# Kernel tuning notes

Measured on AMD Instinct MI355X. Metric: run time of the kernel, lower is better.

The kernel has to match this reference:

```python
import jax, jax.numpy as jnp
import numpy as np

N, E = 50000, 800000
NODE_DIM, HIDDEN, NBASIS = 128, 128, 32


def _mlp(x, w1, b1, w2, b2):
    return jax.nn.silu(x @ w1 + b1) @ w2 + b2


def setup_inputs() -> dict:
    key = jax.random.key(0)
    ks = jax.random.split(key, 16)
    d = {}
    d['h'] = jax.random.normal(ks[0], (N, NODE_DIM), dtype=jnp.float32)
    d['pos'] = jax.random.normal(ks[1], (N, 3), dtype=jnp.float32)
    d['edge_index'] = jax.random.randint(ks[2], (2, E), 0, N, dtype=jnp.int32)
    mlp_in = NODE_DIM * 2 + NBASIS
    def lin(k, fan_in, fan_out):
        bound = 1.0 / np.sqrt(fan_in)
        kw, kb = jax.random.split(k)
        w = jax.random.uniform(kw, (fan_in, fan_out), minval=-bound, maxval=bound, dtype=jnp.float32)
        b = jax.random.uniform(kb, (fan_out,), minval=-bound, maxval=bound, dtype=jnp.float32)
        return w, b
    d['mw1'], d['mb1'] = lin(ks[3], mlp_in, HIDDEN)
    d['mw2'], d['mb2'] = lin(ks[4], HIDDEN, HIDDEN)
    d['nw1'], d['nb1'] = lin(ks[5], NODE_DIM + HIDDEN, HIDDEN)
    d['nw2'], d['nb2'] = lin(ks[6], HIDDEN, NODE_DIM)
    d['cw1'], d['cb1'] = lin(ks[7], HIDDEN, HIDDEN)
    d['cw2'], d['cb2'] = lin(ks[8], HIDDEN, 1)
    return d


def reference(h, pos, edge_index, mw1, mb1, mw2, mb2, nw1, nb1, nw2, nb2, cw1, cb1, cw2, cb2):
    row, col = edge_index[0], edge_index[1]
    # Gaussian smearing constants (start=0, stop=10, num_gaussians=NBASIS)
    offset = jnp.linspace(0.0, 10.0, NBASIS)  # [NBASIS]
    coeff = -0.5 / float(10.0 / (NBASIS - 1)) ** 2

    rel_pos = pos[row] - pos[col]                       # [E, 3]
    sq_dist = jnp.sum(rel_pos ** 2, axis=1, keepdims=True)  # [E, 1]
    dist = jnp.sqrt(sq_dist + 1e-8)                     # [E, 1]
    dist_emb = jnp.exp(coeff * (dist - offset[None, :]) ** 2)  # [E, NBASIS]

    msg_in = jnp.concatenate([h[row], h[col], dist_emb], axis=1)  # [E, 2D+NBASIS]
    messages = _mlp(msg_in, mw1, mb1, mw2, mb2)         # [E, HIDDEN]

    aggr_msgs = jax.ops.segment_sum(messages, row, num_segments=h.shape[0])  # [N, HIDDEN]

    coord_mult = _mlp(messages, cw1, cb1, cw2, cb2)     # [E, 1]
    coord_updates = rel_pos * coord_mult                # [E, 3]
    aggr_coord = jax.ops.segment_sum(coord_updates, row, num_segments=pos.shape[0])
    pos_out = pos + aggr_coord

    node_in = jnp.concatenate([h, aggr_msgs], axis=1)   # [N, D+HIDDEN]
    h_out = h + _mlp(node_in, nw1, nb1, nw2, nb2)
    return (h_out, pos_out)
```

## Files before the change

kernel.cpp:

```cpp
#include <hip/hip_runtime.h>
#include <math.h>

#define N_NODES 50000
#define E_EDGES 800000
#define D 128
#define HID 128
#define NB 32

typedef __attribute__((ext_vector_type(8))) short bf16x8;
typedef __attribute__((ext_vector_type(4))) float f32x4;

#define MW1F 0
#define MW2F 72
#define CW1F 104
#define NW1F 136
#define NW2F 200
#define TOT_KSTEPS 29

__device__ __forceinline__ short f2bf(float f) {
    union { float f; unsigned u; } v; v.f = f;
    unsigned r = v.u + 0x7fffu + ((v.u >> 16) & 1u);
    return (short)(r >> 16);
}
__device__ __forceinline__ float silu_f(float x) { return x / (1.0f + __expf(-x)); }
__device__ __forceinline__ f32x4 splat4(float b) { f32x4 v = {b, b, b, b}; return v; }

__global__ void pack_w(const float* __restrict__ mw1, const float* __restrict__ mw2,
                       const float* __restrict__ cw1, const float* __restrict__ nw1,
                       const float* __restrict__ nw2, short* __restrict__ wp)
{
    const int bid = blockIdx.x;
    const int ks = bid >> 3, nf = bid & 7;
    const int l = threadIdx.x;
    const float* src; int k0;
    if (ks < 9)       { src = mw1; k0 = ks; }
    else if (ks < 13) { src = mw2; k0 = ks - 9; }
    else if (ks < 17) { src = cw1; k0 = ks - 13; }
    else if (ks < 25) { src = nw1; k0 = ks - 17; }
    else              { src = nw2; k0 = ks - 25; }
    bf16x8 pv;
    #pragma unroll
    for (int j = 0; j < 8; ++j)
        pv[j] = f2bf(src[(size_t)(k0 * 32 + (l >> 4) * 8 + j) * 128 + nf * 16 + (l & 15)]);
    *((bf16x8*)wp + (size_t)bid * 64 + l) = pv;
}

#define GEMM2(KSTEPS, STRIDE, WBASE)                                           \
    _Pragma("unroll")                                                          \
    for (int ks = 0; ks < KSTEPS; ++ks) {                                      \
        const int kd = ks * 32 + ag * 8;                                       \
        int b0 = ar * STRIDE + kd * 2;        b0 ^= (ar & 7) << 4;             \
        int b1 = (16 + ar) * STRIDE + kd * 2; b1 ^= (ar & 7) << 4;             \
        bf16x8 a0 = *(const bf16x8*)(sx + b0);                                 \
        bf16x8 a1 = *(const bf16x8*)(sx + b1);                                 \
        const bf16x8* bw = wpv + (size_t)(WBASE + ks * 8) * 64 + l;            \
        _Pragma("unroll")                                                      \
        for (int n = 0; n < 8; ++n) {                                          \
            bf16x8 bb = bw[n * 64];                                            \
            acc0[n] = __builtin_amdgcn_mfma_f32_16x16x32_bf16(a0, bb, acc0[n], 0, 0, 0); \
            acc1[n] = __builtin_amdgcn_mfma_f32_16x16x32_bf16(a1, bb, acc1[n], 0, 0, 0); \
        }                                                                      \
    }

__global__ __launch_bounds__(128, 2) void egnn_edge(
    const float* __restrict__ h, const float* __restrict__ pos,
    const int* __restrict__ ei,
    const float* __restrict__ mb1, const float* __restrict__ mb2,
    const float* __restrict__ cb1, const float* __restrict__ cw2,
    const float* __restrict__ cb2, const short* __restrict__ wp,
    float* __restrict__ aggr_msgs, float* __restrict__ aggr_coord)
{
    __shared__ char sm[2][18432];
    __shared__ int   s_rowm[2][32];
    __shared__ float s_relm[2][32][3];

    const int t = threadIdx.x;
    const int w = t >> 6;
    const int l = t & 63;
    char* sx = sm[w];
    const bf16x8* wpv = (const bf16x8*)wp;
    const int e0 = blockIdx.x * 64 + w * 32;

    {
        const int e_loc = l & 31, half = l >> 5;
        const int ge = e0 + e_loc;
        const int row = ei[ge], col = ei[E_EDGES + ge];
        const float dx = pos[row * 3 + 0] - pos[col * 3 + 0];
        const float dy = pos[row * 3 + 1] - pos[col * 3 + 1];
        const float dz = pos[row * 3 + 2] - pos[col * 3 + 2];
        const float dist = sqrtf(dx * dx + dy * dy + dz * dz + 1e-8f);
        if (half == 0) {
            s_rowm[w][e_loc] = row;
            s_relm[w][e_loc][0] = dx; s_relm[w][e_loc][1] = dy; s_relm[w][e_loc][2] = dz;
        }
        const float GS = 10.0f / 31.0f;
        const float GC = -0.5f / (GS * GS);
        const float* hrow = h + (size_t)row * D;
        const float* hcol = h + (size_t)col * D;
        #pragma unroll
        for (int c = 0; c < 18; ++c) {
            const int k0 = half * 144 + c * 8;
            float v[8];
            if (k0 < 256) {
                const float* src = (k0 < 128) ? (hrow + k0) : (hcol + (k0 - 128));
                float4 va = *(const float4*)src;
                float4 vb = *(const float4*)(src + 4);
                v[0] = va.x; v[1] = va.y; v[2] = va.z; v[3] = va.w;
                v[4] = vb.x; v[5] = vb.y; v[6] = vb.z; v[7] = vb.w;
            } else {
                #pragma unroll
                for (int j = 0; j < 8; ++j) {
                    float dd = dist - (float)(k0 - 256 + j) * GS;
                    v[j] = __expf(GC * dd * dd);
                }
            }
            bf16x8 sv;
            #pragma unroll
            for (int j = 0; j < 8; ++j) sv[j] = f2bf(v[j]);
            int byte = e_loc * 576 + k0 * 2;
            byte ^= (e_loc & 7) << 4;
            *(bf16x8*)(sx + byte) = sv;
        }
    }
    asm volatile("s_waitcnt lgkmcnt(0)" ::: "memory");

    const int ar = l & 15, ag = l >> 4;
    f32x4 acc0[8], acc1[8];

    #pragma unroll
    for (int n = 0; n < 8; ++n) {
        float b = mb1[n * 16 + ar];
        acc0[n] = splat4(b); acc1[n] = splat4(b);
    }
    GEMM2(9, 576, MW1F)

    #pragma unroll
    for (int m = 0; m < 2; ++m)
        #pragma unroll
        for (int n = 0; n < 8; ++n)
            #pragma unroll
            for (int r = 0; r < 4; ++r) {
                float x = (m == 0) ? acc0[n][r] : acc1[n][r];
                const int rw = m * 16 + ag * 4 + r;
                const int cl = n * 16 + ar;
                int byte = rw * 256 + cl * 2;
                byte ^= (rw & 7) << 4;
                *(short*)(sx + byte) = f2bf(silu_f(x));
            }
    asm volatile("s_waitcnt lgkmcnt(0)" ::: "memory");

    #pragma unroll
    for (int n = 0; n < 8; ++n) {
        float b = mb2[n * 16 + ar];
        acc0[n] = splat4(b); acc1[n] = splat4(b);
    }
    GEMM2(4, 256, MW2F)

    int grows[2][4];
    #pragma unroll
    for (int m = 0; m < 2; ++m)
        #pragma unroll
        for (int r = 0; r < 4; ++r)
            grows[m][r] = s_rowm[w][m * 16 + ag * 4 + r];

    #pragma unroll
    for (int m = 0; m < 2; ++m)
        #pragma unroll
        for (int n = 0; n < 8; ++n)
            #pragma unroll
            for (int r = 0; r < 4; ++r) {
                float x = (m == 0) ? acc0[n][r] : acc1[n][r];
                const int rw = m * 16 + ag * 4 + r;
                const int cl = n * 16 + ar;
                int byte = rw * 256 + cl * 2;
                byte ^= (rw & 7) << 4;
                *(short*)(sx + byte) = f2bf(x);
                atomicAdd(&aggr_msgs[(size_t)grows[m][r] * D + cl], x);
            }
    asm volatile("s_waitcnt lgkmcnt(0)" ::: "memory");

    #pragma unroll
    for (int n = 0; n < 8; ++n) {
        float b = cb1[n * 16 + ar];
        acc0[n] = splat4(b); acc1[n] = splat4(b);
    }
    GEMM2(4, 256, CW1F)

    float cw2v[8];
    #pragma unroll
    for (int n = 0; n < 8; ++n) cw2v[n] = cw2[n * 16 + ar];
    float p0[4], p1[4];
    #pragma unroll
    for (int r = 0; r < 4; ++r) {
        float s0 = 0.f, s1 = 0.f;
        #pragma unroll
        for (int n = 0; n < 8; ++n) {
            s0 += silu_f(acc0[n][r]) * cw2v[n];
            s1 += silu_f(acc1[n][r]) * cw2v[n];
        }
        p0[r] = s0; p1[r] = s1;
    }
    #pragma unroll
    for (int off = 1; off < 16; off <<= 1) {
        #pragma unroll
        for (int r = 0; r < 4; ++r) {
            p0[r] += __shfl_xor(p0[r], off);
            p1[r] += __shfl_xor(p1[r], off);
        }
    }
    if (ar == 0) {
        const float cb = cb2[0];
        #pragma unroll
        for (int m = 0; m < 2; ++m)
            #pragma unroll
            for (int r = 0; r < 4; ++r) {
                const int el = m * 16 + ag * 4 + r;
                const float mm = ((m == 0) ? p0[r] : p1[r]) + cb;
                const int gr = grows[m][r];
                atomicAdd(&aggr_coord[gr * 3 + 0], s_relm[w][el][0] * mm);
                atomicAdd(&aggr_coord[gr * 3 + 1], s_relm[w][el][1] * mm);
                atomicAdd(&aggr_coord[gr * 3 + 2], s_relm[w][el][2] * mm);
            }
    }
}

__global__ __launch_bounds__(128, 2) void egnn_node(
    const float* __restrict__ h, const float* __restrict__ aggr,
    const float* __restrict__ nb1, const float* __restrict__ nb2,
    const short* __restrict__ wp, float* __restrict__ out)
{
    __shared__ char sm[2][16384];
    const int t = threadIdx.x, w = t >> 6, l = t & 63;
    char* sx = sm[w];
    const bf16x8* wpv = (const bf16x8*)wp;
    const int n0 = blockIdx.x * 64 + w * 32;

    {
        const int n_loc = l & 31, half = l >> 5;
        int gn = n0 + n_loc; if (gn >= N_NODES) gn = N_NODES - 1;
        const float* src = (half == 0) ? (h + (size_t)gn * D) : (aggr + (size_t)gn * D);
        #pragma unroll
        for (int c = 0; c < 16; ++c) {
            float4 va = *(const float4*)(src + c * 8);
            float4 vb = *(const float4*)(src + c * 8 + 4);
            float v[8] = {va.x, va.y, va.z, va.w, vb.x, vb.y, vb.z, vb.w};
            bf16x8 sv;
            #pragma unroll
            for (int j = 0; j < 8; ++j) sv[j] = f2bf(v[j]);
            int byte = n_loc * 512 + (half * 128 + c * 8) * 2;
            byte ^= (n_loc & 7) << 4;
            *(bf16x8*)(sx + byte) = sv;
        }
    }
    asm volatile("s_waitcnt lgkmcnt(0)" ::: "memory");

    const int ar = l & 15, ag = l >> 4;
    f32x4 acc0[8], acc1[8];

    #pragma unroll
    for (int n = 0; n < 8; ++n) {
        float b = nb1[n * 16 + ar];
        acc0[n] = splat4(b); acc1[n] = splat4(b);
    }
    GEMM2(8, 512, NW1F)

    #pragma unroll
    for (int m = 0; m < 2; ++m)
        #pragma unroll
        for (int n = 0; n < 8; ++n)
            #pragma unroll
            for (int r = 0; r < 4; ++r) {
                float x = (m == 0) ? acc0[n][r] : acc1[n][r];
                const int rw = m * 16 + ag * 4 + r;
                const int cl = n * 16 + ar;
                int byte = rw * 256 + cl * 2;
                byte ^= (rw & 7) << 4;
                *(short*)(sx + byte) = f2bf(silu_f(x));
            }
    asm volatile("s_waitcnt lgkmcnt(0)" ::: "memory");

    #pragma unroll
    for (int n = 0; n < 8; ++n) {
        float b = nb2[n * 16 + ar];
        acc0[n] = splat4(b); acc1[n] = splat4(b);
    }
    GEMM2(4, 256, NW2F)

    #pragma unroll
    for (int m = 0; m < 2; ++m)
        #pragma unroll
        for (int n = 0; n < 8; ++n)
            #pragma unroll
            for (int r = 0; r < 4; ++r) {
                const int rw = m * 16 + ag * 4 + r;
                const int gnode = n0 + rw;
                if (gnode < N_NODES) {
                    const int cl = n * 16 + ar;
                    float x = (m == 0) ? acc0[n][r] : acc1[n][r];
                    out[(size_t)gnode * D + cl] = h[(size_t)gnode * D + cl] + x;
                }
            }
}

__global__ void egnn_pos(const float* __restrict__ pos,
                         const float* __restrict__ aggr_coord,
                         float* __restrict__ pout)
{
    int i = blockIdx.x * 256 + threadIdx.x;
    if (i < N_NODES * 3) pout[i] = pos[i] + aggr_coord[i];
}

extern "C" void kernel_launch(void* const* d_in, const int* in_sizes, int n_in,
                              void* d_out, int out_size, void* d_ws, size_t ws_size,
                              hipStream_t stream)
{
    const float* h   = (const float*)d_in[0];
    const float* pos = (const float*)d_in[1];
    const int*   ei  = (const int*)d_in[2];
    const float* mw1 = (const float*)d_in[3];
    const float* mb1 = (const float*)d_in[4];
    const float* mw2 = (const float*)d_in[5];
    const float* mb2 = (const float*)d_in[6];
    const float* nw1 = (const float*)d_in[7];
    const float* nb1 = (const float*)d_in[8];
    const float* nw2 = (const float*)d_in[9];
    const float* nb2 = (const float*)d_in[10];
    const float* cw1 = (const float*)d_in[11];
    const float* cb1 = (const float*)d_in[12];
    const float* cw2 = (const float*)d_in[13];
    const float* cb2 = (const float*)d_in[14];

    float* out        = (float*)d_out;
    float* aggr_msgs  = (float*)d_ws;
    float* aggr_coord = aggr_msgs + (size_t)N_NODES * D;
    short* wpack      = (short*)(aggr_coord + (size_t)N_NODES * 3);

    hipMemsetAsync(d_ws, 0, (size_t)(N_NODES * D + N_NODES * 3) * sizeof(float), stream);

    pack_w<<<TOT_KSTEPS * 8, 64, 0, stream>>>(mw1, mw2, cw1, nw1, nw2, wpack);

    egnn_edge<<<E_EDGES / 64, 128, 0, stream>>>(
        h, pos, ei, mb1, mb2, cb1, cw2, cb2, wpack, aggr_msgs, aggr_coord);

    egnn_node<<<(N_NODES + 63) / 64, 128, 0, stream>>>(
        h, aggr_msgs, nb1, nb2, wpack, out);

    egnn_pos<<<(N_NODES * 3 + 255) / 256, 256, 0, stream>>>(
        pos, aggr_coord, out + (size_t)N_NODES * D);
}
```

Before: 602.2 us.

## Pre-convert h to bf16 and load MFMA A-fragments directly from global

Adds a kernel that converts node features h to bf16 once. The edge kernel then gathers the row and column feature fragments straight into MFMA A registers and computes the Gaussian basis in registers, with no staging of the 288-wide input through LDS. This halves gather bytes and cuts LDS use, which allows 4 waves per block and higher occupancy. The cost is an extra conversion pass, a larger workspace, and uncoalesced 16-byte gathers issued per fragment.

```diff
diff --git a/kernel.cpp b/kernel.cpp
--- a/kernel.cpp
+++ b/kernel.cpp
@@ -43,6 +43,19 @@
     for (int j = 0; j < 8; ++j)
         pv[j] = f2bf(src[(size_t)(k0 * 32 + (l >> 4) * 8 + j) * 128 + nf * 16 + (l & 15)]);
     *((bf16x8*)wp + (size_t)bid * 64 + l) = pv;
+}
+
+__global__ void conv_h(const float* __restrict__ h, short* __restrict__ hb)
+{
+    int i = blockIdx.x * 256 + threadIdx.x;
+    if (i < N_NODES * D / 8) {
+        float4 va = ((const float4*)h)[i * 2];
+        float4 vb = ((const float4*)h)[i * 2 + 1];
+        bf16x8 o;
+        o[0] = f2bf(va.x); o[1] = f2bf(va.y); o[2] = f2bf(va.z); o[3] = f2bf(va.w);
+        o[4] = f2bf(vb.x); o[5] = f2bf(vb.y); o[6] = f2bf(vb.z); o[7] = f2bf(vb.w);
+        ((bf16x8*)hb)[i] = o;
+    }
 }
 
 #define GEMM2(KSTEPS, STRIDE, WBASE)                                           \
@@ -62,69 +75,47 @@
         }                                                                      \
     }
 
-__global__ __launch_bounds__(128, 2) void egnn_edge(
-    const float* __restrict__ h, const float* __restrict__ pos,
+__global__ __launch_bounds__(256, 4) void egnn_edge(
+    const short* __restrict__ hb, const float* __restrict__ pos,
     const int* __restrict__ ei,
     const float* __restrict__ mb1, const float* __restrict__ mb2,
     const float* __restrict__ cb1, const float* __restrict__ cw2,
     const float* __restrict__ cb2, const short* __restrict__ wp,
     float* __restrict__ aggr_msgs, float* __restrict__ aggr_coord)
 {
-    __shared__ char sm[2][18432];
-    __shared__ int   s_rowm[2][32];
-    __shared__ float s_relm[2][32][3];
+    __shared__ char  sm[4][8192];
+    __shared__ int   s_row[4][32], s_col[4][32];
+    __shared__ float s_dist[4][32];
+    __shared__ float s_rel[4][32][3];
 
     const int t = threadIdx.x;
     const int w = t >> 6;
     const int l = t & 63;
     char* sx = sm[w];
     const bf16x8* wpv = (const bf16x8*)wp;
-    const int e0 = blockIdx.x * 64 + w * 32;
-
-    {
-        const int e_loc = l & 31, half = l >> 5;
-        const int ge = e0 + e_loc;
+    const bf16x8* hbv = (const bf16x8*)hb;
+    const int e0 = blockIdx.x * 128 + w * 32;
+
+    if (l < 32) {
+        const int ge = e0 + l;
         const int row = ei[ge], col = ei[E_EDGES + ge];
         const float dx = pos[row * 3 + 0] - pos[col * 3 + 0];
         const float dy = pos[row * 3 + 1] - pos[col * 3 + 1];
         const float dz = pos[row * 3 + 2] - pos[col * 3 + 2];
         const float dist = sqrtf(dx * dx + dy * dy + dz * dz + 1e-8f);
-        if (half == 0) {
-            s_rowm[w][e_loc] = row;
-            s_relm[w][e_loc][0] = dx; s_relm[w][e_loc][1] = dy; s_relm[w][e_loc][2] = dz;
-        }
-        const float GS = 10.0f / 31.0f;
-        const float GC = -0.5f / (GS * GS);
-        const float* hrow = h + (size_t)row * D;
-        const float* hcol = h + (size_t)col * D;
-        #pragma unroll
-        for (int c = 0; c < 18; ++c) {
-            const int k0 = half * 144 + c * 8;
-            float v[8];
-            if (k0 < 256) {
-                const float* src = (k0 < 128) ? (hrow + k0) : (hcol + (k0 - 128));
-                float4 va = *(const float4*)src;
-                float4 vb = *(const float4*)(src + 4);
-                v[0] = va.x; v[1] = va.y; v[2] = va.z; v[3] = va.w;
-                v[4] = vb.x; v[5] = vb.y; v[6] = vb.z; v[7] = vb.w;
-            } else {
-                #pragma unroll
-                for (int j = 0; j < 8; ++j) {
-                    float dd = dist - (float)(k0 - 256 + j) * GS;
-                    v[j] = __expf(GC * dd * dd);
-                }
-            }
-            bf16x8 sv;
-            #pragma unroll
-            for (int j = 0; j < 8; ++j) sv[j] = f2bf(v[j]);
-            int byte = e_loc * 576 + k0 * 2;
-            byte ^= (e_loc & 7) << 4;
-            *(bf16x8*)(sx + byte) = sv;
-        }
+        s_row[w][l] = row; s_col[w][l] = col; s_dist[w][l] = dist;
+        s_rel[w][l][0] = dx; s_rel[w][l][1] = dy; s_rel[w][l][2] = dz;
     }
     asm volatile("s_waitcnt lgkmcnt(0)" ::: "memory");
 
     const int ar = l & 15, ag = l >> 4;
+    const int row0 = s_row[w][ar],      col0 = s_col[w][ar];
+    const int row1 = s_row[w][16 + ar], col1 = s_col[w][16 + ar];
+    const float d0 = s_dist[w][ar], d1 = s_dist[w][16 + ar];
+
+    const float GS = 10.0f / 31.0f;
+    const float GC = -0.5f / (GS * GS);
+
     f32x4 acc0[8], acc1[8];
 
     #pragma unroll
@@ -132,7 +123,32 @@
         float b = mb1[n * 16 + ar];
         acc0[n] = splat4(b); acc1[n] = splat4(b);
     }
-    GEMM2(9, 576, MW1F)
+    #pragma unroll
+    for (int ks = 0; ks < 9; ++ks) {
+        bf16x8 a0, a1;
+        if (ks < 4) {
+            a0 = hbv[(size_t)row0 * 16 + ks * 4 + ag];
+            a1 = hbv[(size_t)row1 * 16 + ks * 4 + ag];
+        } else if (ks < 8) {
+            a0 = hbv[(size_t)col0 * 16 + (ks - 4) * 4 + ag];
+            a1 = hbv[(size_t)col1 * 16 + (ks - 4) * 4 + ag];
+        } else {
+            #pragma unroll
+            for (int j = 0; j < 8; ++j) {
+                const float g = (float)(ag * 8 + j) * GS;
+                const float dd0 = d0 - g, dd1 = d1 - g;
+                a0[j] = f2bf(__expf(GC * dd0 * dd0));
+                a1[j] = f2bf(__expf(GC * dd1 * dd1));
+            }
+        }
+        const bf16x8* bw = wpv + (size_t)(MW1F + ks * 8) * 64 + l;
+        #pragma unroll
+        for (int n = 0; n < 8; ++n) {
+            bf16x8 bb = bw[n * 64];
+            acc0[n] = __builtin_amdgcn_mfma_f32_16x16x32_bf16(a0, bb, acc0[n], 0, 0, 0);
+            acc1[n] = __builtin_amdgcn_mfma_f32_16x16x32_bf16(a1, bb, acc1[n], 0, 0, 0);
+        }
+    }
 
     #pragma unroll
     for (int m = 0; m < 2; ++m)
@@ -161,7 +177,7 @@
     for (int m = 0; m < 2; ++m)
         #pragma unroll
         for (int r = 0; r < 4; ++r)
-            grows[m][r] = s_rowm[w][m * 16 + ag * 4 + r];
+            grows[m][r] = s_row[w][m * 16 + ag * 4 + r];
 
     #pragma unroll
     for (int m = 0; m < 2; ++m)
@@ -217,9 +233,9 @@
                 const int el = m * 16 + ag * 4 + r;
                 const float mm = ((m == 0) ? p0[r] : p1[r]) + cb;
                 const int gr = grows[m][r];
-                atomicAdd(&aggr_coord[gr * 3 + 0], s_relm[w][el][0] * mm);
-                atomicAdd(&aggr_coord[gr * 3 + 1], s_relm[w][el][1] * mm);
-                atomicAdd(&aggr_coord[gr * 3 + 2], s_relm[w][el][2] * mm);
+                atomicAdd(&aggr_coord[gr * 3 + 0], s_rel[w][el][0] * mm);
+                atomicAdd(&aggr_coord[gr * 3 + 1], s_rel[w][el][1] * mm);
+                atomicAdd(&aggr_coord[gr * 3 + 2], s_rel[w][el][2] * mm);
             }
     }
 }
@@ -334,13 +350,15 @@
     float* aggr_msgs  = (float*)d_ws;
     float* aggr_coord = aggr_msgs + (size_t)N_NODES * D;
     short* wpack      = (short*)(aggr_coord + (size_t)N_NODES * 3);
+    short* hb         = wpack + (size_t)TOT_KSTEPS * 8 * 64 * 8;
 
     hipMemsetAsync(d_ws, 0, (size_t)(N_NODES * D + N_NODES * 3) * sizeof(float), stream);
 
     pack_w<<<TOT_KSTEPS * 8, 64, 0, stream>>>(mw1, mw2, cw1, nw1, nw2, wpack);
-
-    egnn_edge<<<E_EDGES / 64, 128, 0, stream>>>(
-        h, pos, ei, mb1, mb2, cb1, cw2, cb2, wpack, aggr_msgs, aggr_coord);
+    conv_h<<<(N_NODES * D / 8 + 255) / 256, 256, 0, stream>>>(h, hb);
+
+    egnn_edge<<<E_EDGES / 128, 256, 0, stream>>>(
+        hb, pos, ei, mb1, mb2, cb1, cw2, cb2, wpack, aggr_msgs, aggr_coord);
 
     egnn_node<<<(N_NODES + 63) / 64, 128, 0, stream>>>(
         h, aggr_msgs, nb1, nb2, wpack, out);
```

Result: slower. 709.0 us (+17.7%).
